# Kernel optimization log

Measured on AMD Instinct MI355X. Metric: run time of the kernel, lower is better.

## Reference

```python
import jax, jax.numpy as jnp
import numpy as np

TOP_K = 2
POOL = 4  # EfficientSpatialRouter.pool_scale


def silu(v):
    return v * jax.nn.sigmoid(v)


def setup_inputs() -> dict:
    key = jax.random.key(0)
    ks = jax.random.split(key, 6)
    B, C, H, W = 16, 256, 56, 56
    E, O = 4, 256
    hidden = 2 * C            # SimpleExpert expand_ratio=2
    red = max(C // 8, 8)      # router reduced_channels
    x = jax.random.normal(ks[0], (B, C, H, W), jnp.float32)
    router_w1 = jax.random.normal(ks[1], (red, C, 3, 3), jnp.float32) * 0.02
    router_w2 = jax.random.normal(ks[2], (E, red), jnp.float32) * 0.01
    expert_w1 = jax.random.normal(ks[3], (E, hidden, C), jnp.float32) * 0.05
    expert_w2 = jax.random.normal(ks[4], (E, O, hidden), jnp.float32) * 0.03
    shared_w = jax.random.normal(ks[5], (O, C), jnp.float32) * 0.05
    return {"x": x, "router_w1": router_w1, "router_w2": router_w2,
            "expert_w1": expert_w1, "expert_w2": expert_w2, "shared_w": shared_w}


def reference(x, router_w1, router_w2, expert_w1, expert_w2, shared_w):
    # Eval mode: no router noise; BatchNorm with default running stats
    # (mean=0, var=1, gamma=1, beta=0) is the identity, so BNs are omitted.
    B, C, H, W = x.shape
    E = router_w2.shape[0]

    # --- EfficientSpatialRouter ---
    xp = x.reshape(B, C, H // POOL, POOL, W // POOL, POOL).mean(axis=(3, 5))
    h = jax.lax.conv_general_dilated(
        xp, router_w1, window_strides=(1, 1), padding=((1, 1), (1, 1)),
        dimension_numbers=("NCHW", "OIHW", "NCHW"))
    h = silu(h)  # [B, red, H/4, W/4]
    # 1x1 conv to E channels then spatial mean == mean of per-pixel logits
    logits = jnp.einsum("er,brij->be", router_w2, h) / (h.shape[2] * h.shape[3])
    probs = jax.nn.softmax(logits, axis=1)
    topv, topi = jax.lax.top_k(probs, TOP_K)          # [B,k]
    topv = topv / (topv.sum(axis=1, keepdims=True) + 1e-6)

    # --- shared expert (1x1 conv + BN(id) + SiLU) ---
    shared = silu(jnp.einsum("oc,bcij->boij", shared_w, x))

    # --- all SimpleExperts densely (1x1 conv -> SiLU -> 1x1 conv) ---
    hid = silu(jnp.einsum("edc,bcij->bedij", expert_w1, x))   # [B,E,hid,H,W]
    eo = jnp.einsum("eod,bedij->beoij", expert_w2, hid)       # [B,E,O,H,W]

    # --- weighted combine of top-k experts ---
    wdense = jnp.zeros((B, E), x.dtype).at[jnp.arange(B)[:, None], topi].add(topv)
    expert_out = jnp.einsum("be,beoij->boij", wdense, eo)
    return shared + expert_out
```

## Files before the change

### kernel.cpp

```cpp
#include <hip/hip_runtime.h>
#include <hip/hip_bf16.h>

typedef __attribute__((ext_vector_type(8))) short bf16x8;
typedef __attribute__((ext_vector_type(16))) float f32x16;
typedef __attribute__((ext_vector_type(4))) unsigned short ushort4v;

__device__ __forceinline__ unsigned short f2bf(float f) {
  unsigned u = __float_as_uint(f);
  return (unsigned short)((u + 0x7FFFu + ((u >> 16) & 1u)) >> 16);
}
__device__ __forceinline__ float silu_f(float v) { return v / (1.f + __expf(-v)); }

__global__ void pack_k(const float* __restrict__ shw, const float* __restrict__ ew1,
                       const float* __restrict__ ew2, unsigned short* __restrict__ wshp,
                       unsigned short* __restrict__ w1p, unsigned short* __restrict__ w2p) {
  int idx = blockIdx.x * 256 + threadIdx.x;
  if (idx < 65536) {
    int j = idx;
    int i = j & 7, l = (j >> 3) & 63, ks = (j >> 9) & 15, rb = j >> 13;
    int row = rb * 32 + (l & 31), k = ks * 16 + (l >> 5) * 8 + i;
    wshp[j] = f2bf(shw[row * 256 + k]);
  } else if (idx < 589824) {
    int j = idx - 65536;
    int i = j & 7, l = (j >> 3) & 63, ks = (j >> 9) & 15, rb = (j >> 13) & 15, e = j >> 17;
    int row = rb * 32 + (l & 31), k = ks * 16 + (l >> 5) * 8 + i;
    w1p[j] = f2bf(ew1[((size_t)e * 512 + row) * 256 + k]);
  } else if (idx < 1114112) {
    int j = idx - 589824;
    int i = j & 7, l = (j >> 3) & 63, ks = (j >> 9) & 31, rb = (j >> 14) & 7, e = j >> 17;
    int row = rb * 32 + (l & 31), k = ks * 16 + (l >> 5) * 8 + i;
    w2p[j] = f2bf(ew2[((size_t)e * 256 + row) * 512 + k]);
  }
}

__global__ void pool_k(const float* __restrict__ x, float* __restrict__ xp) {
  int idx = blockIdx.x * 256 + threadIdx.x;
  if (idx >= 16 * 256 * 196) return;
  int pj = idx % 14, tmp = idx / 14, pi = tmp % 14, bc = tmp / 14;
  const float* src = x + (size_t)bc * 3136 + pi * 4 * 56 + pj * 4;
  float s = 0.f;
#pragma unroll
  for (int u = 0; u < 4; ++u) {
    float4 v = *reinterpret_cast<const float4*>(src + u * 56);
    s += v.x + v.y + v.z + v.w;
  }
  xp[idx] = s * 0.0625f;
}

__global__ __launch_bounds__(256) void router_conv_k(const float* __restrict__ xp,
                                                     const float* __restrict__ rw1,
                                                     float* __restrict__ hsum) {
  const int b = blockIdx.x >> 5, r = blockIdx.x & 31;
  __shared__ float wl[2304];
  __shared__ float xl[32][256];
  __shared__ float red[4];
  const int t = threadIdx.x;
  for (int i = t; i < 2304; i += 256) wl[i] = rw1[r * 2304 + i];
  for (int i = t; i < 32 * 256; i += 256) (&xl[0][0])[i] = 0.f;
  const int pi = t / 14, pj = t % 14;
  float acc = 0.f;
  for (int cc = 0; cc < 8; ++cc) {
    __syncthreads();
    for (int i = t; i < 32 * 196; i += 256) {
      int c = i / 196, px = i % 196;
      xl[c][(px / 14 + 1) * 16 + (px % 14 + 1)] =
          xp[((size_t)b * 256 + cc * 32 + c) * 196 + px];
    }
    __syncthreads();
    if (t < 196) {
      for (int c = 0; c < 32; ++c) {
        const float* wp = &wl[(cc * 32 + c) * 9];
        const float* xc = &xl[c][pi * 16 + pj];
#pragma unroll
        for (int u = 0; u < 3; ++u)
#pragma unroll
          for (int v = 0; v < 3; ++v) acc += xc[u * 16 + v] * wp[u * 3 + v];
      }
    }
  }
  float s = (t < 196) ? silu_f(acc) : 0.f;
#pragma unroll
  for (int off = 32; off > 0; off >>= 1) s += __shfl_down(s, off);
  if ((t & 63) == 0) red[t >> 6] = s;
  __syncthreads();
  if (t == 0) hsum[b * 32 + r] = red[0] + red[1] + red[2] + red[3];
}

__global__ void topk_k(const float* __restrict__ hsum, const float* __restrict__ rw2,
                       float* __restrict__ selv, int* __restrict__ sele) {
  const int t = threadIdx.x;
  const int b = t >> 2, e = t & 3;
  float l = 0.f;
#pragma unroll
  for (int r = 0; r < 32; ++r) l += rw2[e * 32 + r] * hsum[b * 32 + r];
  l *= (1.f / 196.f);
  float m = fmaxf(l, __shfl_xor(l, 1));
  m = fmaxf(m, __shfl_xor(m, 2));
  float p = __expf(l - m);
  float sm = p + __shfl_xor(p, 1);
  sm += __shfl_xor(sm, 2);
  float prob = p / sm;
  float p0 = __shfl(prob, (b << 2) | 0);
  float p1 = __shfl(prob, (b << 2) | 1);
  float p2 = __shfl(prob, (b << 2) | 2);
  float p3 = __shfl(prob, (b << 2) | 3);
  if (e == 0) {
    float pr[4] = {p0, p1, p2, p3};
    int i1 = 0;
    for (int i = 1; i < 4; ++i)
      if (pr[i] > pr[i1]) i1 = i;
    int i2 = (i1 == 0) ? 1 : 0;
    for (int i = 0; i < 4; ++i) {
      if (i == i1 || i == i2) continue;
      if (pr[i] > pr[i2]) i2 = i;
    }
    float denom = pr[i1] + pr[i2] + 1e-6f;
    selv[b * 2 + 0] = pr[i1] / denom;
    selv[b * 2 + 1] = pr[i2] / denom;
    sele[b * 2 + 0] = i1;
    sele[b * 2 + 1] = i2;
  }
}

__global__ __launch_bounds__(512, 4) void moe_main_k(
    const float* __restrict__ x, const unsigned short* __restrict__ wshp,
    const unsigned short* __restrict__ w1p, const unsigned short* __restrict__ w2p,
    const float* __restrict__ selv, const int* __restrict__ sele,
    float* __restrict__ out) {
  constexpr int C = 256, HW = 3136;
  __shared__ __align__(16) unsigned short xs[64 * 256];
  __shared__ __align__(16) unsigned short hs[64 * 256];

  const int bx = blockIdx.x;
  const int b = bx / 49, tile = bx - b * 49;
  const int px0 = tile * 64;
  const int t = threadIdx.x;
  const int w = t >> 6, l = t & 63;
  const int l31 = l & 31, lh = l >> 5;

  {
    const int px = l;
    const float* xb = x + (size_t)b * C * HW + px0 + px;
#pragma unroll
    for (int cg = 0; cg < 4; ++cg) {
      const int ch0 = w * 32 + cg * 8;
      alignas(16) unsigned short tmp[8];
#pragma unroll
      for (int i2 = 0; i2 < 8; ++i2) tmp[i2] = f2bf(xb[(size_t)(ch0 + i2) * HW]);
      const int idx = (px * 256 + ch0) ^ ((px & 7) << 3);
      *reinterpret_cast<bf16x8*>(&xs[idx]) = *reinterpret_cast<const bf16x8*>(tmp);
    }
  }

  f32x16 oacc[2];
#pragma unroll
  for (int cf = 0; cf < 2; ++cf)
#pragma unroll
    for (int r = 0; r < 16; ++r) oacc[cf][r] = 0.f;

  __syncthreads();

  {
    const unsigned short* A = wshp + (size_t)(w * 16) * 512 + l * 8;
#pragma unroll
    for (int ks = 0; ks < 16; ++ks) {
      const bf16x8 afr = *reinterpret_cast<const bf16x8*>(A + ks * 512);
#pragma unroll
      for (int cf = 0; cf < 2; ++cf) {
        const int px = cf * 32 + l31;
        const int idx = (px * 256 + ks * 16 + lh * 8) ^ ((px & 7) << 3);
        const bf16x8 bfr = *reinterpret_cast<const bf16x8*>(&xs[idx]);
        oacc[cf] = __builtin_amdgcn_mfma_f32_32x32x16_bf16(afr, bfr, oacc[cf], 0, 0, 0);
      }
    }
  }
#pragma unroll
  for (int cf = 0; cf < 2; ++cf)
#pragma unroll
    for (int r = 0; r < 16; ++r) oacc[cf][r] = silu_f(oacc[cf][r]);

#pragma unroll 1
  for (int ei = 0; ei < 2; ++ei) {
    const int e = sele[b * 2 + ei];
    const float v = selv[b * 2 + ei];
#pragma unroll 1
    for (int ph = 0; ph < 2; ++ph) {
      f32x16 hacc[2];
#pragma unroll
      for (int cf = 0; cf < 2; ++cf)
#pragma unroll
        for (int r = 0; r < 16; ++r) hacc[cf][r] = 0.f;
      const unsigned short* A1 = w1p + (size_t)((e * 16 + ph * 8 + w) * 16) * 512 + l * 8;
#pragma unroll
      for (int ks = 0; ks < 16; ++ks) {
        const bf16x8 afr = *reinterpret_cast<const bf16x8*>(A1 + ks * 512);
#pragma unroll
        for (int cf = 0; cf < 2; ++cf) {
          const int px = cf * 32 + l31;
          const int idx = (px * 256 + ks * 16 + lh * 8) ^ ((px & 7) << 3);
          const bf16x8 bfr = *reinterpret_cast<const bf16x8*>(&xs[idx]);
          hacc[cf] = __builtin_amdgcn_mfma_f32_32x32x16_bf16(afr, bfr, hacc[cf], 0, 0, 0);
        }
      }
      __syncthreads();
#pragma unroll
      for (int cf = 0; cf < 2; ++cf) {
        const int px = cf * 32 + l31;
#pragma unroll
        for (int g = 0; g < 4; ++g) {
          alignas(8) unsigned short pk[4];
#pragma unroll
          for (int j = 0; j < 4; ++j) pk[j] = f2bf(v * silu_f(hacc[cf][g * 4 + j]));
          const int kk = w * 32 + g * 8 + lh * 4;
          const int idx = (px * 256 + kk) ^ ((px & 7) << 3);
          *reinterpret_cast<ushort4v*>(&hs[idx]) = *reinterpret_cast<const ushort4v*>(pk);
        }
      }
      __syncthreads();
      const unsigned short* A2 = w2p + (size_t)((e * 8 + w) * 32 + ph * 16) * 512 + l * 8;
#pragma unroll
      for (int ks = 0; ks < 16; ++ks) {
        const bf16x8 afr = *reinterpret_cast<const bf16x8*>(A2 + ks * 512);
#pragma unroll
        for (int cf = 0; cf < 2; ++cf) {
          const int px = cf * 32 + l31;
          const int idx = (px * 256 + ks * 16 + lh * 8) ^ ((px & 7) << 3);
          const bf16x8 bfr = *reinterpret_cast<const bf16x8*>(&hs[idx]);
          oacc[cf] = __builtin_amdgcn_mfma_f32_32x32x16_bf16(afr, bfr, oacc[cf], 0, 0, 0);
        }
      }
    }
  }

#pragma unroll
  for (int cf = 0; cf < 2; ++cf) {
    const int px = px0 + cf * 32 + l31;
#pragma unroll
    for (int g = 0; g < 4; ++g) {
#pragma unroll
      for (int j = 0; j < 4; ++j) {
        const int o = w * 32 + g * 8 + 4 * lh + j;
        out[((size_t)b * 256 + o) * HW + px] = oacc[cf][g * 4 + j];
      }
    }
  }
}

extern "C" void kernel_launch(void* const* d_in, const int* in_sizes, int n_in,
                              void* d_out, int out_size, void* d_ws, size_t ws_size,
                              hipStream_t stream) {
  const float* x = (const float*)d_in[0];
  const float* rw1 = (const float*)d_in[1];
  const float* rw2 = (const float*)d_in[2];
  const float* ew1 = (const float*)d_in[3];
  const float* ew2 = (const float*)d_in[4];
  const float* shw = (const float*)d_in[5];
  float* out = (float*)d_out;
  char* ws = (char*)d_ws;

  float* xp = (float*)(ws);
  float* hsum = (float*)(ws + 3211264);
  float* selv = (float*)(ws + 3213312);
  int* sele = (int*)(ws + 3213440);
  unsigned short* wshp = (unsigned short*)(ws + 3213568);
  unsigned short* w1p = wshp + 65536;
  unsigned short* w2p = w1p + 524288;

  pack_k<<<4352, 256, 0, stream>>>(shw, ew1, ew2, wshp, w1p, w2p);
  pool_k<<<3136, 256, 0, stream>>>(x, xp);
  router_conv_k<<<512, 256, 0, stream>>>(xp, rw1, hsum);
  topk_k<<<1, 64, 0, stream>>>(hsum, rw2, selv, sele);
  moe_main_k<<<784, 512, 0, stream>>>(x, wshp, w1p, w2p, selv, sele, out);
}
```

Measured before the change: 184.4 us.

## Use 2x2 MFMA register tiles with 4 waves and merge pack/pool kernels

The main MoE kernel now runs 4 waves per block instead of 8. Each wave computes a 2x2 grid of 32x32 MFMA tiles, so each A and B fragment load is reused twice. The GEMM inner loop is double-buffered in registers, and the LDS layout changes from swizzled row-major to a k-group-major layout. The weight pack and pooling kernels are merged into one launch to save launch overhead. The larger accumulator footprint raises register pressure, and the new LDS layout may introduce bank conflicts.

```diff
diff --git a/kernel.cpp b/kernel.cpp
--- a/kernel.cpp
+++ b/kernel.cpp
@@ -5,46 +5,48 @@
 typedef __attribute__((ext_vector_type(16))) float f32x16;
 typedef __attribute__((ext_vector_type(4))) unsigned short ushort4v;
 
-__device__ __forceinline__ unsigned short f2bf(float f) {
+static __device__ __forceinline__ unsigned short f2bf(float f) {
   unsigned u = __float_as_uint(f);
   return (unsigned short)((u + 0x7FFFu + ((u >> 16) & 1u)) >> 16);
 }
-__device__ __forceinline__ float silu_f(float v) { return v / (1.f + __expf(-v)); }
-
-__global__ void pack_k(const float* __restrict__ shw, const float* __restrict__ ew1,
-                       const float* __restrict__ ew2, unsigned short* __restrict__ wshp,
-                       unsigned short* __restrict__ w1p, unsigned short* __restrict__ w2p) {
-  int idx = blockIdx.x * 256 + threadIdx.x;
-  if (idx < 65536) {
-    int j = idx;
-    int i = j & 7, l = (j >> 3) & 63, ks = (j >> 9) & 15, rb = j >> 13;
-    int row = rb * 32 + (l & 31), k = ks * 16 + (l >> 5) * 8 + i;
-    wshp[j] = f2bf(shw[row * 256 + k]);
-  } else if (idx < 589824) {
-    int j = idx - 65536;
-    int i = j & 7, l = (j >> 3) & 63, ks = (j >> 9) & 15, rb = (j >> 13) & 15, e = j >> 17;
-    int row = rb * 32 + (l & 31), k = ks * 16 + (l >> 5) * 8 + i;
-    w1p[j] = f2bf(ew1[((size_t)e * 512 + row) * 256 + k]);
-  } else if (idx < 1114112) {
-    int j = idx - 589824;
-    int i = j & 7, l = (j >> 3) & 63, ks = (j >> 9) & 31, rb = (j >> 14) & 7, e = j >> 17;
-    int row = rb * 32 + (l & 31), k = ks * 16 + (l >> 5) * 8 + i;
-    w2p[j] = f2bf(ew2[((size_t)e * 256 + row) * 512 + k]);
-  }
-}
-
-__global__ void pool_k(const float* __restrict__ x, float* __restrict__ xp) {
-  int idx = blockIdx.x * 256 + threadIdx.x;
-  if (idx >= 16 * 256 * 196) return;
-  int pj = idx % 14, tmp = idx / 14, pi = tmp % 14, bc = tmp / 14;
-  const float* src = x + (size_t)bc * 3136 + pi * 4 * 56 + pj * 4;
-  float s = 0.f;
-#pragma unroll
-  for (int u = 0; u < 4; ++u) {
-    float4 v = *reinterpret_cast<const float4*>(src + u * 56);
-    s += v.x + v.y + v.z + v.w;
-  }
-  xp[idx] = s * 0.0625f;
+static __device__ __forceinline__ float silu_f(float v) { return v / (1.f + __expf(-v)); }
+
+__global__ void prep_k(const float* __restrict__ shw, const float* __restrict__ ew1,
+                       const float* __restrict__ ew2, const float* __restrict__ x,
+                       unsigned short* __restrict__ wshp, unsigned short* __restrict__ w1p,
+                       unsigned short* __restrict__ w2p, float* __restrict__ xp) {
+  const int bid = blockIdx.x;
+  if (bid < 4352) {
+    int idx = bid * 256 + threadIdx.x;
+    if (idx < 65536) {
+      int j = idx;
+      int i = j & 7, l = (j >> 3) & 63, ks = (j >> 9) & 15, rb = j >> 13;
+      int row = rb * 32 + (l & 31), k = ks * 16 + (l >> 5) * 8 + i;
+      wshp[j] = f2bf(shw[row * 256 + k]);
+    } else if (idx < 589824) {
+      int j = idx - 65536;
+      int i = j & 7, l = (j >> 3) & 63, ks = (j >> 9) & 15, rb = (j >> 13) & 15, e = j >> 17;
+      int row = rb * 32 + (l & 31), k = ks * 16 + (l >> 5) * 8 + i;
+      w1p[j] = f2bf(ew1[((size_t)e * 512 + row) * 256 + k]);
+    } else if (idx < 1114112) {
+      int j = idx - 589824;
+      int i = j & 7, l = (j >> 3) & 63, ks = (j >> 9) & 31, rb = (j >> 14) & 7, e = j >> 17;
+      int row = rb * 32 + (l & 31), k = ks * 16 + (l >> 5) * 8 + i;
+      w2p[j] = f2bf(ew2[((size_t)e * 256 + row) * 512 + k]);
+    }
+  } else {
+    int idx = (bid - 4352) * 256 + threadIdx.x;
+    if (idx >= 16 * 256 * 196) return;
+    int pj = idx % 14, tmp = idx / 14, pi = tmp % 14, bc = tmp / 14;
+    const float* src = x + (size_t)bc * 3136 + pi * 4 * 56 + pj * 4;
+    float s = 0.f;
+#pragma unroll
+    for (int u = 0; u < 4; ++u) {
+      float4 v = *reinterpret_cast<const float4*>(src + u * 56);
+      s += v.x + v.y + v.z + v.w;
+    }
+    xp[idx] = s * 0.0625f;
+  }
 }
 
 __global__ __launch_bounds__(256) void router_conv_k(const float* __restrict__ xp,
@@ -122,62 +124,90 @@
   }
 }
 
-__global__ __launch_bounds__(512, 4) void moe_main_k(
+static __device__ __forceinline__ void gemm_k256(
+    const unsigned short* __restrict__ A0, const unsigned short* __restrict__ A1,
+    const unsigned short* B0, const unsigned short* B1, f32x16 acc[2][2]) {
+  bf16x8 aA[2], bA[2], aB[2], bB[2];
+  aA[0] = *reinterpret_cast<const bf16x8*>(A0);
+  aA[1] = *reinterpret_cast<const bf16x8*>(A1);
+  bA[0] = *reinterpret_cast<const bf16x8*>(B0);
+  bA[1] = *reinterpret_cast<const bf16x8*>(B1);
+#pragma unroll
+  for (int kk = 0; kk < 16; kk += 2) {
+    aB[0] = *reinterpret_cast<const bf16x8*>(A0 + (kk + 1) * 512);
+    aB[1] = *reinterpret_cast<const bf16x8*>(A1 + (kk + 1) * 512);
+    bB[0] = *reinterpret_cast<const bf16x8*>(B0 + (kk + 1) * 1024);
+    bB[1] = *reinterpret_cast<const bf16x8*>(B1 + (kk + 1) * 1024);
+    acc[0][0] = __builtin_amdgcn_mfma_f32_32x32x16_bf16(aA[0], bA[0], acc[0][0], 0, 0, 0);
+    acc[0][1] = __builtin_amdgcn_mfma_f32_32x32x16_bf16(aA[0], bA[1], acc[0][1], 0, 0, 0);
+    acc[1][0] = __builtin_amdgcn_mfma_f32_32x32x16_bf16(aA[1], bA[0], acc[1][0], 0, 0, 0);
+    acc[1][1] = __builtin_amdgcn_mfma_f32_32x32x16_bf16(aA[1], bA[1], acc[1][1], 0, 0, 0);
+    if (kk + 2 < 16) {
+      aA[0] = *reinterpret_cast<const bf16x8*>(A0 + (kk + 2) * 512);
+      aA[1] = *reinterpret_cast<const bf16x8*>(A1 + (kk + 2) * 512);
+      bA[0] = *reinterpret_cast<const bf16x8*>(B0 + (kk + 2) * 1024);
+      bA[1] = *reinterpret_cast<const bf16x8*>(B1 + (kk + 2) * 1024);
+    }
+    acc[0][0] = __builtin_amdgcn_mfma_f32_32x32x16_bf16(aB[0], bB[0], acc[0][0], 0, 0, 0);
+    acc[0][1] = __builtin_amdgcn_mfma_f32_32x32x16_bf16(aB[0], bB[1], acc[0][1], 0, 0, 0);
+    acc[1][0] = __builtin_amdgcn_mfma_f32_32x32x16_bf16(aB[1], bB[0], acc[1][0], 0, 0, 0);
+    acc[1][1] = __builtin_amdgcn_mfma_f32_32x32x16_bf16(aB[1], bB[1], acc[1][1], 0, 0, 0);
+  }
+}
+
+__global__ __launch_bounds__(256, 2) void moe_main_k(
     const float* __restrict__ x, const unsigned short* __restrict__ wshp,
     const unsigned short* __restrict__ w1p, const unsigned short* __restrict__ w2p,
     const float* __restrict__ selv, const int* __restrict__ sele,
     float* __restrict__ out) {
-  constexpr int C = 256, HW = 3136;
-  __shared__ __align__(16) unsigned short xs[64 * 256];
-  __shared__ __align__(16) unsigned short hs[64 * 256];
-
-  const int bx = blockIdx.x;
-  const int b = bx / 49, tile = bx - b * 49;
+  constexpr int HW = 3136;
+  __shared__ __align__(16) unsigned short xs[32 * 64 * 8];
+  __shared__ __align__(16) unsigned short hs[32 * 64 * 8];
+
+  const int b = blockIdx.x / 49, tile = blockIdx.x - b * 49;
   const int px0 = tile * 64;
   const int t = threadIdx.x;
   const int w = t >> 6, l = t & 63;
   const int l31 = l & 31, lh = l >> 5;
 
   {
-    const int px = l;
-    const float* xb = x + (size_t)b * C * HW + px0 + px;
-#pragma unroll
-    for (int cg = 0; cg < 4; ++cg) {
-      const int ch0 = w * 32 + cg * 8;
+    const float* xb = x + (size_t)b * 256 * HW + px0 + l;
+#pragma unroll
+    for (int cg = 0; cg < 8; ++cg) {
+      const int c0 = w * 64 + cg * 8;
       alignas(16) unsigned short tmp[8];
 #pragma unroll
-      for (int i2 = 0; i2 < 8; ++i2) tmp[i2] = f2bf(xb[(size_t)(ch0 + i2) * HW]);
-      const int idx = (px * 256 + ch0) ^ ((px & 7) << 3);
-      *reinterpret_cast<bf16x8*>(&xs[idx]) = *reinterpret_cast<const bf16x8*>(tmp);
-    }
-  }
-
-  f32x16 oacc[2];
-#pragma unroll
-  for (int cf = 0; cf < 2; ++cf)
-#pragma unroll
-    for (int r = 0; r < 16; ++r) oacc[cf][r] = 0.f;
+      for (int i = 0; i < 8; ++i) tmp[i] = f2bf(xb[(size_t)(c0 + i) * HW]);
+      *reinterpret_cast<bf16x8*>(&xs[((c0 >> 3) * 64 + l) * 8]) =
+          *reinterpret_cast<const bf16x8*>(tmp);
+    }
+  }
+
+  const unsigned short* xB0 = xs + (lh * 64 + l31) * 8;
+  const unsigned short* xB1 = xB0 + 32 * 8;
+  const unsigned short* hB0 = hs + (lh * 64 + l31) * 8;
+  const unsigned short* hB1 = hB0 + 32 * 8;
+
+  f32x16 oacc[2][2];
+#pragma unroll
+  for (int i = 0; i < 2; ++i)
+#pragma unroll
+    for (int j = 0; j < 2; ++j)
+#pragma unroll
+      for (int r = 0; r < 16; ++r) oacc[i][j][r] = 0.f;
 
   __syncthreads();
 
   {
-    const unsigned short* A = wshp + (size_t)(w * 16) * 512 + l * 8;
-#pragma unroll
-    for (int ks = 0; ks < 16; ++ks) {
-      const bf16x8 afr = *reinterpret_cast<const bf16x8*>(A + ks * 512);
-#pragma unroll
-      for (int cf = 0; cf < 2; ++cf) {
-        const int px = cf * 32 + l31;
-        const int idx = (px * 256 + ks * 16 + lh * 8) ^ ((px & 7) << 3);
-        const bf16x8 bfr = *reinterpret_cast<const bf16x8*>(&xs[idx]);
-        oacc[cf] = __builtin_amdgcn_mfma_f32_32x32x16_bf16(afr, bfr, oacc[cf], 0, 0, 0);
-      }
-    }
-  }
-#pragma unroll
-  for (int cf = 0; cf < 2; ++cf)
-#pragma unroll
-    for (int r = 0; r < 16; ++r) oacc[cf][r] = silu_f(oacc[cf][r]);
+    const unsigned short* A0 = wshp + (size_t)(w * 2) * 16 * 512 + l * 8;
+    gemm_k256(A0, A0 + 8192, xB0, xB1, oacc);
+  }
+#pragma unroll
+  for (int i = 0; i < 2; ++i)
+#pragma unroll
+    for (int j = 0; j < 2; ++j)
+#pragma unroll
+      for (int r = 0; r < 16; ++r) oacc[i][j][r] = silu_f(oacc[i][j][r]);
 
 #pragma unroll 1
   for (int ei = 0; ei < 2; ++ei) {
@@ -185,65 +215,52 @@
     const float v = selv[b * 2 + ei];
 #pragma unroll 1
     for (int ph = 0; ph < 2; ++ph) {
-      f32x16 hacc[2];
-#pragma unroll
-      for (int cf = 0; cf < 2; ++cf)
-#pragma unroll
-        for (int r = 0; r < 16; ++r) hacc[cf][r] = 0.f;
-      const unsigned short* A1 = w1p + (size_t)((e * 16 + ph * 8 + w) * 16) * 512 + l * 8;
-#pragma unroll
-      for (int ks = 0; ks < 16; ++ks) {
-        const bf16x8 afr = *reinterpret_cast<const bf16x8*>(A1 + ks * 512);
+      f32x16 hacc[2][2];
+#pragma unroll
+      for (int i = 0; i < 2; ++i)
+#pragma unroll
+        for (int j = 0; j < 2; ++j)
+#pragma unroll
+          for (int r = 0; r < 16; ++r) hacc[i][j][r] = 0.f;
+      {
+        const unsigned short* A0 =
+            w1p + (size_t)(e * 16 + ph * 8 + w * 2) * 16 * 512 + l * 8;
+        gemm_k256(A0, A0 + 8192, xB0, xB1, hacc);
+      }
+      __syncthreads();
+#pragma unroll
+      for (int rfi = 0; rfi < 2; ++rfi)
 #pragma unroll
         for (int cf = 0; cf < 2; ++cf) {
-          const int px = cf * 32 + l31;
-          const int idx = (px * 256 + ks * 16 + lh * 8) ^ ((px & 7) << 3);
-          const bf16x8 bfr = *reinterpret_cast<const bf16x8*>(&xs[idx]);
-          hacc[cf] = __builtin_amdgcn_mfma_f32_32x32x16_bf16(afr, bfr, hacc[cf], 0, 0, 0);
+#pragma unroll
+          for (int g = 0; g < 4; ++g) {
+            alignas(8) unsigned short pk[4];
+#pragma unroll
+            for (int j = 0; j < 4; ++j)
+              pk[j] = f2bf(v * silu_f(hacc[rfi][cf][g * 4 + j]));
+            const int kg = w * 8 + rfi * 4 + g;
+            const int ui = (kg * 64 + cf * 32 + l31) * 8 + lh * 4;
+            *reinterpret_cast<ushort4v*>(&hs[ui]) = *reinterpret_cast<const ushort4v*>(pk);
+          }
         }
-      }
       __syncthreads();
-#pragma unroll
-      for (int cf = 0; cf < 2; ++cf) {
-        const int px = cf * 32 + l31;
-#pragma unroll
-        for (int g = 0; g < 4; ++g) {
-          alignas(8) unsigned short pk[4];
-#pragma unroll
-          for (int j = 0; j < 4; ++j) pk[j] = f2bf(v * silu_f(hacc[cf][g * 4 + j]));
-          const int kk = w * 32 + g * 8 + lh * 4;
-          const int idx = (px * 256 + kk) ^ ((px & 7) << 3);
-          *reinterpret_cast<ushort4v*>(&hs[idx]) = *reinterpret_cast<const ushort4v*>(pk);
-        }
-      }
-      __syncthreads();
-      const unsigned short* A2 = w2p + (size_t)((e * 8 + w) * 32 + ph * 16) * 512 + l * 8;
-#pragma unroll
-      for (int ks = 0; ks < 16; ++ks) {
-        const bf16x8 afr = *reinterpret_cast<const bf16x8*>(A2 + ks * 512);
-#pragma unroll
-        for (int cf = 0; cf < 2; ++cf) {
-          const int px = cf * 32 + l31;
-          const int idx = (px * 256 + ks * 16 + lh * 8) ^ ((px & 7) << 3);
-          const bf16x8 bfr = *reinterpret_cast<const bf16x8*>(&hs[idx]);
-          oacc[cf] = __builtin_amdgcn_mfma_f32_32x32x16_bf16(afr, bfr, oacc[cf], 0, 0, 0);
-        }
-      }
-    }
-  }
-
-#pragma unroll
-  for (int cf = 0; cf < 2; ++cf) {
-    const int px = px0 + cf * 32 + l31;
-#pragma unroll
-    for (int g = 0; g < 4; ++g) {
-#pragma unroll
-      for (int j = 0; j < 4; ++j) {
-        const int o = w * 32 + g * 8 + 4 * lh + j;
-        out[((size_t)b * 256 + o) * HW + px] = oacc[cf][g * 4 + j];
-      }
-    }
-  }
+      {
+        const unsigned short* A0 =
+            w2p + ((size_t)(e * 8 + w * 2) * 32 + ph * 16) * 512 + l * 8;
+        gemm_k256(A0, A0 + 16384, hB0, hB1, oacc);
+      }
+    }
+  }
+
+#pragma unroll
+  for (int rfi = 0; rfi < 2; ++rfi)
+#pragma unroll
+    for (int cf = 0; cf < 2; ++cf)
+#pragma unroll
+      for (int r = 0; r < 16; ++r) {
+        const int o = w * 64 + rfi * 32 + (r & 3) + 8 * (r >> 2) + 4 * lh;
+        out[((size_t)b * 256 + o) * HW + px0 + cf * 32 + l31] = oacc[rfi][cf][r];
+      }
 }
 
 extern "C" void kernel_launch(void* const* d_in, const int* in_sizes, int n_in,
@@ -266,9 +283,8 @@
   unsigned short* w1p = wshp + 65536;
   unsigned short* w2p = w1p + 524288;
 
-  pack_k<<<4352, 256, 0, stream>>>(shw, ew1, ew2, wshp, w1p, w2p);
-  pool_k<<<3136, 256, 0, stream>>>(x, xp);
+  prep_k<<<7488, 256, 0, stream>>>(shw, ew1, ew2, x, wshp, w1p, w2p, xp);
   router_conv_k<<<512, 256, 0, stream>>>(xp, rw1, hsum);
   topk_k<<<1, 64, 0, stream>>>(hsum, rw2, selv, sele);
-  moe_main_k<<<784, 512, 0, stream>>>(x, wshp, w1p, w2p, selv, sele, out);
-}
+  moe_main_k<<<784, 256, 0, stream>>>(x, wshp, w1p, w2p, selv, sele, out);
+}
```

After: 168.8 us. 8.5% less time.
